# Optimization experiments

Hardware: AMD Instinct MI355X
Metric: run time of the kernel (lower is better)

The kernel has to match this reference:

```python
import jax, jax.numpy as jnp
import numpy as np

L = 4          # num_layers
H = 128        # hidden_channels
F = 128        # num_filters
G = 25         # num_gaussians
N = 10000      # nodes
E = 320000     # radius-graph edges
EH = 40000     # hull edges
NG = 64        # graphs in batch
CUTOFF = 5.0
PI = float(np.pi)
LOG2 = float(np.log(2.0))


def ssp(x):  # ShiftedSoftplus
    return jax.nn.softplus(x) - LOG2


def setup_inputs() -> dict:
    key = jax.random.key(0)
    ks = iter(jax.random.split(key, 64))
    w = lambda shape: jax.random.normal(next(ks), shape, jnp.float32) * 0.05
    inp = {
        'z': jax.random.randint(next(ks), (N,), 0, 100),
        'edge_index': jax.random.randint(next(ks), (2, E), 0, N),
        'edge_index_hull': jax.random.randint(next(ks), (2, EH), 0, N),
        'batch': jnp.sort(jax.random.randint(next(ks), (N,), 0, NG)),
        'dist': jax.random.uniform(next(ks), (E,), jnp.float32) * CUTOFF,
        'fea_hull': jax.random.normal(next(ks), (EH, 7), jnp.float32),
        'emb_table': w((100, H)),
        'lin_w': w((L, F, H)),
        'mlp_w1': w((L, F, G)), 'mlp_b1': jnp.zeros((L, F), jnp.float32),
        'mlp_w2': w((L, F, F)), 'mlp_b2': jnp.zeros((L, F), jnp.float32),
        'linh_w': w((L, F, H)),
        'mlph_w1': w((L, F, 7)), 'mlph_b1': jnp.zeros((L, F), jnp.float32),
        'mlph_w2': w((L, F, F)), 'mlph_b2': jnp.zeros((L, F), jnp.float32),
        'v1_w': w((L, H, F)), 'v1_b': jnp.zeros((L, H), jnp.float32),
        'v2_w': w((L, 64, H)), 'v2_b': jnp.zeros((L, 64), jnp.float32),
        'vh1_w': w((L, H, F)), 'vh1_b': jnp.zeros((L, H), jnp.float32),
        'vh2_w': w((L, 64, H)), 'vh2_b': jnp.zeros((L, 64), jnp.float32),
        'cat_w': w((L, H, 128)), 'cat_b': jnp.zeros((L, H), jnp.float32),
        'u1_w': w((64, H)), 'u1_b': jnp.zeros((64,), jnp.float32),
        'u2_w': w((1, 64)), 'u2_b': jnp.zeros((1,), jnp.float32),
    }
    return inp


def reference(z, edge_index, edge_index_hull, batch, dist, fea_hull, emb_table,
              lin_w, mlp_w1, mlp_b1, mlp_w2, mlp_b2,
              linh_w, mlph_w1, mlph_b1, mlph_w2, mlph_b2,
              v1_w, v1_b, v2_w, v2_b, vh1_w, vh1_b, vh2_w, vh2_b,
              cat_w, cat_b, u1_w, u1_b, u2_w, u2_b):
    n = z.shape[0]
    # Gaussian distance embedding: emb(0, cutoff, G)
    offset = jnp.linspace(0.0, CUTOFF, G)
    coeff = -0.5 / (offset[1] - offset[0]) ** 2
    dist_emb = jnp.exp(coeff * (dist[:, None] - offset[None, :]) ** 2)  # [E,G]
    C = 0.5 * (jnp.cos(dist * PI / CUTOFF) + 1.0)                       # [E]
    j, i = edge_index[0], edge_index[1]
    jh, ih = edge_index_hull[0], edge_index_hull[1]
    v = emb_table[z]                                                    # [N,H]
    for l in range(L):
        # update_e
        W = (ssp(dist_emb @ mlp_w1[l].T + mlp_b1[l]) @ mlp_w2[l].T + mlp_b2[l]) * C[:, None]
        e = (v @ lin_w[l].T)[j] * W                                     # [E,F]
        Wh = ssp(fea_hull @ mlph_w1[l].T + mlph_b1[l]) @ mlph_w2[l].T + mlph_b2[l]
        eh = (v @ linh_w[l].T)[jh] * Wh                                 # [EH,F]
        # update_v
        out = jax.ops.segment_sum(e, i, num_segments=n)
        out = ssp(out @ v1_w[l].T + v1_b[l]) @ v2_w[l].T + v2_b[l]      # [N,64]
        outh = jax.ops.segment_sum(eh, ih, num_segments=n)
        outh = ssp(outh @ vh1_w[l].T + vh1_b[l]) @ vh2_w[l].T + vh2_b[l]
        v = v + ssp(jnp.concatenate([out, outh], axis=1) @ cat_w[l].T + cat_b[l])
    # update_u
    u = ssp(v @ u1_w.T + u1_b) @ u2_w.T + u2_b                          # [N,1]
    return jax.ops.segment_sum(u, batch, num_segments=NG)               # [NG,1]
```

## Files before the change

### kernel.cpp

```cpp
#include <hip/hip_runtime.h>
#include <hip/hip_bf16.h>

typedef __hip_bfloat16 bf16;
typedef unsigned short ushort;
typedef __attribute__((ext_vector_type(8))) short short8;
typedef __attribute__((ext_vector_type(4))) float f32x4;

__device__ __forceinline__ float dssp(float x){
  return fmaxf(x, 0.f) + __logf(1.f + __expf(-fabsf(x))) - 0.693147180559945f;
}
__device__ __forceinline__ int clampi(int x, int lo, int hi){ return x<lo?lo:(x>hi?hi:x); }
__device__ __forceinline__ ushort f2b(float f){
  unsigned x = __float_as_uint(f);
  return (ushort)((x + 0x7fffu + ((x>>16)&1u)) >> 16);
}
__device__ __forceinline__ float b2f16(ushort u){ return __uint_as_float(((unsigned)u)<<16); }

constexpr int TBL_K    = 4096;
constexpr int TBL_ROWS = TBL_K + 1;
constexpr int TBL_T16  = (TBL_ROWS + 15) / 16;

struct Seg { const void* src; float* dst; int n; };
struct SegTable { Seg s[18]; int count; long total; };
struct WSeg { const void* src; ushort* dst; int n; };
struct WTable { WSeg s[10]; int count; int total; };

__global__ void setup_all(const unsigned* __restrict__ raw, int* flag,
                          int* cnt_r, int* cnt_h, float* uacc,
                          int2* spk_r, int2* spk_h, int N, int E, int EH){
  __shared__ int c;
  int t = blockIdx.x*blockDim.x + threadIdx.x;
  if (t < N){ cnt_r[t]=0; cnt_h[t]=0; }
  if (t < 64) uacc[t]=0.f;
  if (t < E)  spk_r[t]=make_int2(0,0);
  if (t < EH) spk_h[t]=make_int2(0,0);
  if (blockIdx.x==0){
    if (threadIdx.x==0) c=0;
    __syncthreads();
    unsigned u  = raw[threadIdx.x];
    unsigned lo = u & 0xFFFFu;
    int e = (int)((lo >> 7) & 0xFF);
    int ok = (lo==0u) || (e >= 0x70 && e <= 0x8F);
    atomicAdd(&c, ok);
    __syncthreads();
    if (threadIdx.x==0) *flag = (c >= 160) ? 1 : 0;
  }
}

__global__ __launch_bounds__(256) void convert_count(SegTable tbl, WTable wt,
    const int* __restrict__ flag,
    const int* __restrict__ ei, const int* __restrict__ eih,
    int E, int EH, int N, int* cnt_r, int* cnt_h, int CA, int CB){
  int b = blockIdx.x;
  if (b < CA){
    int mode = *flag;
    long tid    = (long)b*256 + threadIdx.x;
    long stride = (long)CA*256;
    for (long i=tid; i<tbl.total; i+=stride){
      long off = i; int k = 0;
      while (k < tbl.count-1 && off >= tbl.s[k].n){ off -= tbl.s[k].n; k++; }
      float f;
      if (mode) f = __bfloat162float(((const bf16*)tbl.s[k].src)[off]);
      else      f = ((const float*)tbl.s[k].src)[off];
      tbl.s[k].dst[off] = (f==f) ? f : 0.f;
    }
  } else if (b < CA+CB){
    int mode = *flag;
    long tid    = (long)(b-CA)*256 + threadIdx.x;
    long stride = (long)CB*256;
    for (long i=tid; i<wt.total; i+=stride){
      long off = i; int k = 0;
      while (k < wt.count-1 && off >= wt.s[k].n){ off -= wt.s[k].n; k++; }
      if (mode) wt.s[k].dst[off] = ((const ushort*)wt.s[k].src)[off];
      else {
        float f = ((const float*)wt.s[k].src)[off];
        wt.s[k].dst[off] = f2b((f==f)? f : 0.f);
      }
    }
  } else {
    int t = (b-CA-CB)*256 + threadIdx.x;
    if (t < E)  atomicAdd(&cnt_r[clampi(ei[E + t], 0, N-1)], 1);
    if (t < EH) atomicAdd(&cnt_h[clampi(eih[EH + t], 0, N-1)], 1);
  }
}

__global__ __launch_bounds__(1024) void scan_pair(const int* cnt_r, int* off_r, int* cur_r,
                                                  const int* cnt_h, int* off_h, int* cur_h, int N){
  __shared__ int s[1024];
  int t = threadIdx.x;
  int CH = (N + 1023) / 1024;
  for (int which=0; which<2; which++){
    const int* cnt = which? cnt_h : cnt_r;
    int* off = which? off_h : off_r;
    int* cur = which? cur_h : cur_r;
    int base = t*CH;
    int sum = 0;
    for (int q=0;q<CH;q++){ int idx=base+q; sum += (idx<N)? cnt[idx] : 0; }
    __syncthreads();
    s[t]=sum; __syncthreads();
    for (int ofs=1; ofs<1024; ofs<<=1){
      int v = s[t]; int vp = (t>=ofs)? s[t-ofs] : 0;
      __syncthreads(); s[t]=v+vp; __syncthreads();
    }
    int run = (t>0)? s[t-1] : 0;
    for (int q=0;q<CH;q++){
      int idx=base+q;
      if (idx<N){ off[idx]=run; cur[idx]=run; run += cnt[idx]; }
    }
    if (t==1023) off[N] = s[1023];
  }
}

__global__ void scatter_edges(const int* __restrict__ ei, const float* __restrict__ distc,
                              const int* __restrict__ eih, int E, int EH, int N,
                              int* cur_r, int* cur_h, int2* spk_r, int2* spk_h){
  int t = blockIdx.x*blockDim.x + threadIdx.x;
  if (t < E){
    int i = clampi(ei[E+t], 0, N-1);
    int p = clampi(atomicAdd(&cur_r[i], 1), 0, E-1);
    float x = fminf(fmaxf(distc[t]*(4096.0f/5.0f), 0.f), 4095.999f);
    int i0 = (int)x; if (i0 > TBL_K-1) i0 = TBL_K-1;
    unsigned fr16 = (unsigned)((x - (float)i0)*65536.0f); if (fr16 > 65535u) fr16 = 65535u;
    spk_r[p] = make_int2(clampi(ei[t],0,N-1), (int)(((unsigned)i0<<16)|fr16));
  }
  if (t < EH){
    int ih = clampi(eih[EH+t], 0, N-1);
    int p = clampi(atomicAdd(&cur_h[ih], 1), 0, EH-1);
    spk_h[p] = make_int2(clampi(eih[t],0,N-1), t);
  }
}

__device__ __forceinline__ short8 afragb(const ushort (*Xb)[136], int lane, int k0){
  int m=lane&15, q=(lane>>4)&3;
  return *(const short8*)(&Xb[m][k0+q*8]);
}
__device__ __forceinline__ short8 bfrag(const ushort* __restrict__ W, int cbase, int lane, int k0){
  int n=lane&15, q=(lane>>4)&3;
  return *(const short8*)(W + (size_t)(cbase+n)*128 + k0 + q*8);
}
template<int NT>
__device__ __forceinline__ void mgemm(const ushort (*Xb)[136],
    const ushort* __restrict__ W, int t, f32x4 d[NT]){
  int lane=t&63, w=t>>6;
  #pragma unroll
  for (int ct=0;ct<NT;ct++) d[ct]=(f32x4){0.f,0.f,0.f,0.f};
  #pragma unroll
  for (int kc=0;kc<4;kc++){
    short8 a = afragb(Xb, lane, kc*32);
    #pragma unroll
    for (int ct=0;ct<NT;ct++){
      short8 b = bfrag(W, w*(NT*16)+ct*16, lane, kc*32);
      d[ct] = __builtin_amdgcn_mfma_f32_16x16x32_bf16(a, b, d[ct], 0, 0, 0);
    }
  }
}
template<int NT>
__device__ __forceinline__ void d2tile(ushort (*Y)[136], const f32x4 d[NT], int t,
    int colofs, const float* __restrict__ bias, int do_ssp){
  int lane=t&63, w=t>>6, q=(lane>>4)&3, n=lane&15;
  #pragma unroll
  for (int ct=0;ct<NT;ct++){
    int c = w*(NT*16)+ct*16+n;
    float bv = bias? bias[c] : 0.f;
    #pragma unroll
    for (int i=0;i<4;i++){
      float y = d[ct][i] + bv;
      if (do_ssp) y = dssp(y);
      Y[q*4+i][colofs+c] = f2b(y);
    }
  }
}
template<int NT>
__device__ __forceinline__ void d2os(float (*Os)[132], const f32x4 d[NT], int t,
    const float* __restrict__ bias, int do_ssp){
  int lane=t&63, w=t>>6, q=(lane>>4)&3, n=lane&15;
  #pragma unroll
  for (int ct=0;ct<NT;ct++){
    int c = w*(NT*16)+ct*16+n;
    float bv = bias? bias[c] : 0.f;
    #pragma unroll
    for (int i=0;i<4;i++){
      float y = d[ct][i] + bv;
      if (do_ssp) y = dssp(y);
      Os[q*4+i][c] = y;
    }
  }
}
__device__ __forceinline__ void d2glob_c(ushort* __restrict__ out, const f32x4 d[2],
    int t, int row0, int N, ushort (*Tmp)[136]){
  d2tile<2>(Tmp, d, t, 0, nullptr, 0);
  __syncthreads();
  int r=t>>4, o=(t&15)*8;
  int gr=row0+r;
  if (gr<N) *(uint4*)(out + (size_t)gr*128 + o) = *(const uint4*)&Tmp[r][o];
  __syncthreads();
}

__global__ __launch_bounds__(256) void build_wtab_mfma(
    const float* __restrict__ mlp_w1, const float* __restrict__ mlp_b1,
    const ushort* __restrict__ mlp_w2b, const float* __restrict__ mlp_b2,
    ushort* __restrict__ Wtab){
  int l    = blockIdx.x / TBL_T16;
  int tile = blockIdx.x % TBL_T16;
  int row0 = tile * 16;
  const float* w1 = mlp_w1 + l*128*25;
  const float* b1 = mlp_b1 + l*128;
  const ushort* w2 = mlp_w2b + (size_t)l*16384;
  const float* b2 = mlp_b2 + l*128;
  __shared__ float  Gs[16][26];
  __shared__ ushort Xb[16][136];
  __shared__ ushort Tb[16][136];
  int t = threadIdx.x;
  for (int idx=t; idx<16*25; idx+=256){
    int r=idx/25, k=idx%25;
    float dd = (row0+r) * (5.0f/4096.0f);
    float x  = dd - (float)k*(5.0f/24.0f);
    Gs[r][k] = __expf(-11.52f*x*x);
  }
  __syncthreads();
  {
    int r = t>>4, c0 = (t&15)*8;
    float fv[25];
    #pragma unroll
    for (int k=0;k<25;k++) fv[k]=Gs[r][k];
    short8 pk;
    #pragma unroll
    for (int j=0;j<8;j++){
      int c=c0+j;
      float s=b1[c];
      #pragma unroll
      for (int k=0;k<25;k++) s=fmaf(fv[k], w1[c*25+k], s);
      pk[j]=(short)f2b(dssp(s));
    }
    *(short8*)&Xb[r][c0]=pk;
  }
  __syncthreads();
  f32x4 d[2];
  mgemm<2>(Xb, w2, t, d);
  {
    int lane=t&63, w=t>>6, q=(lane>>4)&3, n=lane&15;
    #pragma unroll
    for (int ct=0;ct<2;ct++){
      int c=w*32+ct*16+n;
      float bv=b2[c];
      #pragma unroll
      for (int i=0;i<4;i++){
        int gr=row0+q*4+i;
        float dd = gr*(5.0f/4096.0f);
        float Cf = 0.5f*(cosf(dd*(3.14159265358979f/5.0f))+1.0f);
        Tb[q*4+i][c]=f2b((d[ct][i]+bv)*Cf);
      }
    }
  }
  __syncthreads();
  int r=t>>4, o=(t&15)*8;
  int gr=row0+r;
  if (gr<TBL_ROWS)
    *(uint4*)(Wtab + ((size_t)l*TBL_ROWS+gr)*128 + o) = *(const uint4*)&Tb[r][o];
}

__device__ void hull_body(int bid, const int2* __restrict__ spk_h,
    const float* __restrict__ fea,
    const float* __restrict__ mlph_w1, const float* __restrict__ mlph_b1,
    const ushort* __restrict__ mlph_w2b, const float* __restrict__ mlph_b2,
    ushort* __restrict__ WhS_base, size_t lstride,
    int EH, int tilesPerLayer, int l0, char* smem){
  int l    = l0 + bid / tilesPerLayer;
  int tile = bid % tilesPerLayer;
  int row0 = tile*64;
  const float* w1 = mlph_w1 + l*128*7;
  const float* b1 = mlph_b1 + l*128;
  const ushort* w2 = mlph_w2b + (size_t)l*16384;
  const float* b2 = mlph_b2 + l*128;
  ushort* WhS = WhS_base + (size_t)(l-l0)*lstride;
  int*   Eid = (int*)smem;
  float (*Fs)[8] = (float(*)[8])(smem+256);
  ushort (*Buf)[136] = (ushort(*)[136])(smem+2304);
  int t=threadIdx.x;
  if (t < 64){
    int p=row0+t;
    Eid[t]=(p<EH)? clampi(spk_h[p].y,0,EH-1):0;
  }
  __syncthreads();
  for (int idx=t; idx<448; idx+=256){
    int r=idx/7, k=idx%7;
    int p=row0+r;
    Fs[r][k]=(p<EH)? fea[(size_t)Eid[r]*7+k]:0.f;
  }
  __syncthreads();
  {
    int c0=(t&31)*4, r0=(t>>5)*8;
    float w[4][7]; float bb[4];
    #pragma unroll
    for (int cc=0;cc<4;cc++){
      bb[cc]=b1[c0+cc];
      #pragma unroll
      for (int k=0;k<7;k++) w[cc][k]=w1[(c0+cc)*7+k];
    }
    #pragma unroll
    for (int rr=0;rr<8;rr++){
      int r=r0+rr;
      float fv[7];
      #pragma unroll
      for (int k=0;k<7;k++) fv[k]=Fs[r][k];
      ushort o[4];
      #pragma unroll
      for (int cc=0;cc<4;cc++){
        float s=bb[cc];
        #pragma unroll
        for (int k=0;k<7;k++) s=fmaf(fv[k],w[cc][k],s);
        o[cc]=f2b(dssp(s));
      }
      unsigned lo=(unsigned)o[0]|((unsigned)o[1]<<16);
      unsigned hi=(unsigned)o[2]|((unsigned)o[3]<<16);
      *(uint2*)&Buf[r][c0]=make_uint2(lo,hi);
    }
  }
  __syncthreads();
  int lane=t&63, w=t>>6;
  const ushort (*Xw)[136] = (const ushort (*)[136])&Buf[w*16][0];
  f32x4 d[8];
  #pragma unroll
  for (int ct=0;ct<8;ct++) d[ct]=(f32x4){0.f,0.f,0.f,0.f};
  #pragma unroll
  for (int kc=0;kc<4;kc++){
    short8 a = afragb(Xw, lane, kc*32);
    #pragma unroll
    for (int ct=0;ct<8;ct++){
      short8 b = bfrag(w2, ct*16, lane, kc*32);
      d[ct] = __builtin_amdgcn_mfma_f32_16x16x32_bf16(a, b, d[ct], 0, 0, 0);
    }
  }
  __syncthreads();
  int q=(lane>>4)&3, n=lane&15;
  #pragma unroll
  for (int ct=0;ct<8;ct++){
    int c=ct*16+n;
    float bv=b2[c];
    #pragma unroll
    for (int i=0;i<4;i++)
      Buf[w*16+q*4+i][c] = f2b(d[ct][i]+bv);
  }
  __syncthreads();
  #pragma unroll
  for (int j=0;j<4;j++){
    int idx=j*256+t;
    int r=idx>>4, o=(idx&15)*8;
    *(uint4*)(WhS + (size_t)(row0+r)*128 + o) = *(const uint4*)&Buf[r][o];
  }
}

__device__ void f_first_body(int bid, const int* __restrict__ z,
    const float* __restrict__ emb, float* __restrict__ v,
    const ushort* __restrict__ linA, const ushort* __restrict__ linB,
    ushort* __restrict__ vlin, ushort* __restrict__ vlinh, int N, char* smem){
  ushort (*Xb)[136] = (ushort(*)[136])smem;
  ushort (*Tb)[136] = (ushort(*)[136])(smem+4352);
  int t=threadIdx.x; int row0=bid*16;
  f32x4 d[2];
  for (int idx=t; idx<512; idx+=256){
    int r=idx>>5, k4=(idx&31)*4; int gr=row0+r;
    int zz=(gr<N)? clampi(z[gr],0,99):0;
    float4 f = *(const float4*)(emb + (size_t)zz*128 + k4);
    unsigned r0 = (unsigned)f2b(f.x) | ((unsigned)f2b(f.y)<<16);
    unsigned r1 = (unsigned)f2b(f.z) | ((unsigned)f2b(f.w)<<16);
    *(uint2*)&Xb[r][k4] = make_uint2(r0,r1);
    if (gr<N) *(float4*)(v + (size_t)gr*128 + k4) = f;
  }
  __syncthreads();
  mgemm<2>(Xb, linA, t, d);
  d2glob_c(vlin, d, t, row0, N, Tb);
  mgemm<2>(Xb, linB, t, d);
  d2glob_c(vlinh, d, t, row0, N, Tb);
}

__global__ __launch_bounds__(256) void hull_pack_first(const int2* __restrict__ spk_h,
    const float* __restrict__ fea,
    const float* __restrict__ mlph_w1, const float* __restrict__ mlph_b1,
    const ushort* __restrict__ mlph_w2b, const float* __restrict__ mlph_b2,
    ushort* __restrict__ WhS, size_t lstride, int EH, int ht64,
    const int* __restrict__ z, const float* __restrict__ emb, float* __restrict__ v,
    const ushort* __restrict__ linA, const ushort* __restrict__ linB,
    ushort* __restrict__ vlin, ushort* __restrict__ vlinh, int N, int nt,
    const ushort* __restrict__ Wtab, unsigned* __restrict__ Wpk, int PB, int HB){
  __shared__ __align__(16) char smem[19968];
  int b = blockIdx.x;
  if (b < HB){
    hull_body(b, spk_h, fea, mlph_w1, mlph_b1, mlph_w2b, mlph_b2,
              WhS, lstride, EH, ht64, 0, smem);
  } else if (b < HB+nt){
    f_first_body(b-HB, z, emb, v, linA, linB, vlin, vlinh, N, smem);
  } else {
    long tid    = (long)(b-HB-nt)*256 + threadIdx.x;
    long stride = (long)PB*256;
    const long TOT = 4L*TBL_K*128;
    for (long i=tid; i<TOT; i+=stride){
      int l = (int)(i / ((long)TBL_K*128));
      long rem = i % ((long)TBL_K*128);
      int r = (int)(rem >> 7), f = (int)(rem & 127);
      const ushort* base = Wtab + (size_t)l*TBL_ROWS*128;
      Wpk[i] = (((unsigned)base[(size_t)(r+1)*128+f])<<16) | (unsigned)base[(size_t)r*128+f];
    }
  }
}

__global__ __launch_bounds__(256) void hull_all(const int2* __restrict__ spk_h,
    const float* __restrict__ fea,
    const float* __restrict__ mlph_w1, const float* __restrict__ mlph_b1,
    const ushort* __restrict__ mlph_w2b, const float* __restrict__ mlph_b2,
    ushort* __restrict__ WhS_base, size_t lstride,
    int EH, int tilesPerLayer, int l0){
  __shared__ __align__(16) char smem[19968];
  hull_body(blockIdx.x, spk_h, fea, mlph_w1, mlph_b1, mlph_w2b, mlph_b2,
            WhS_base, lstride, EH, tilesPerLayer, l0, smem);
}

__global__ __launch_bounds__(256) void f_mid(
    const float* __restrict__ accR, const float* __restrict__ accH,
    float* __restrict__ v,
    const ushort* __restrict__ v1w, const float* __restrict__ v1b,
    const ushort* __restrict__ v2w, const float* __restrict__ v2b,
    const ushort* __restrict__ vh1w, const float* __restrict__ vh1b,
    const ushort* __restrict__ vh2w, const float* __restrict__ vh2b,
    const ushort* __restrict__ cw, const float* __restrict__ cb,
    const ushort* __restrict__ linA, const ushort* __restrict__ linB,
    ushort* __restrict__ vlin, ushort* __restrict__ vlinh, int N){
  __shared__ ushort Xb[16][136];
  __shared__ ushort Xb2[16][136];
  __shared__ ushort Xb3[16][136];
  __shared__ float  Os[16][132];
  int t=threadIdx.x; int row0=blockIdx.x*16;
  f32x4 d[2]; f32x4 d1[1];

  for (int path=0; path<2; path++){
    const float* X = path? accH : accR;
    __syncthreads();
    for (int idx=t; idx<512; idx+=256){
      int r=idx>>5, k4=(idx&31)*4; int gr=row0+r;
      float4 f=(gr<N)? *(const float4*)(X+(size_t)gr*128+k4):make_float4(0,0,0,0);
      unsigned r0 = (unsigned)f2b(f.x) | ((unsigned)f2b(f.y)<<16);
      unsigned r1 = (unsigned)f2b(f.z) | ((unsigned)f2b(f.w)<<16);
      *(uint2*)&Xb[r][k4] = make_uint2(r0,r1);
    }
    __syncthreads();
    mgemm<2>(Xb, path?vh1w:v1w, t, d);
    d2tile<2>(Xb2, d, t, 0, path?vh1b:v1b, 1);
    __syncthreads();
    mgemm<1>(Xb2, path?vh2w:v2w, t, d1);
    d2tile<1>(Xb3, d1, t, path*64, path?vh2b:v2b, 0);
  }
  __syncthreads();
  mgemm<2>(Xb3, cw, t, d);
  d2os<2>(Os, d, t, cb, 1);
  __syncthreads();
  for (int idx=t; idx<512; idx+=256){
    int r=idx>>5, k4=(idx&31)*4; int gr=row0+r;
    float4 f=(gr<N)? *(const float4*)(v+(size_t)gr*128+k4):make_float4(0,0,0,0);
    f.x+=Os[r][k4]; f.y+=Os[r][k4+1]; f.z+=Os[r][k4+2]; f.w+=Os[r][k4+3];
    if (gr<N) *(float4*)(v+(size_t)gr*128+k4)=f;
    unsigned r0 = (unsigned)f2b(f.x) | ((unsigned)f2b(f.y)<<16);
    unsigned r1 = (unsigned)f2b(f.z) | ((unsigned)f2b(f.w)<<16);
    *(uint2*)&Xb[r][k4] = make_uint2(r0,r1);
  }
  __syncthreads();
  mgemm<2>(Xb, linA, t, d);
  d2glob_c(vlin, d, t, row0, N, Xb2);
  mgemm<2>(Xb, linB, t, d);
  d2glob_c(vlinh, d, t, row0, N, Xb2);
}

__global__ __launch_bounds__(256) void f_last(
    const float* __restrict__ accR, const float* __restrict__ accH,
    const float* __restrict__ v,
    const ushort* __restrict__ v1w, const float* __restrict__ v1b,
    const ushort* __restrict__ v2w, const float* __restrict__ v2b,
    const ushort* __restrict__ vh1w, const float* __restrict__ vh1b,
    const ushort* __restrict__ vh2w, const float* __restrict__ vh2b,
    const ushort* __restrict__ cw, const float* __restrict__ cb,
    const ushort* __restrict__ u1w, const float* __restrict__ u1b,
    const float* __restrict__ u2w, const float* __restrict__ u2b,
    const int* __restrict__ batch, float* __restrict__ uacc, int N){
  __shared__ ushort Xb[16][136];
  __shared__ ushort Xb2[16][136];
  __shared__ ushort Xb3[16][136];
  __shared__ float  Os[16][132];
  __shared__ float ss[16];
  __shared__ int   bb[16];
  int t=threadIdx.x; int row0=blockIdx.x*16;
  f32x4 d[2]; f32x4 d1[1];

  for (int path=0; path<2; path++){
    const float* X = path? accH : accR;
    __syncthreads();
    for (int idx=t; idx<512; idx+=256){
      int r=idx>>5, k4=(idx&31)*4; int gr=row0+r;
      float4 f=(gr<N)? *(const float4*)(X+(size_t)gr*128+k4):make_float4(0,0,0,0);
      unsigned r0 = (unsigned)f2b(f.x) | ((unsigned)f2b(f.y)<<16);
      unsigned r1 = (unsigned)f2b(f.z) | ((unsigned)f2b(f.w)<<16);
      *(uint2*)&Xb[r][k4] = make_uint2(r0,r1);
    }
    __syncthreads();
    mgemm<2>(Xb, path?vh1w:v1w, t, d);
    d2tile<2>(Xb2, d, t, 0, path?vh1b:v1b, 1);
    __syncthreads();
    mgemm<1>(Xb2, path?vh2w:v2w, t, d1);
    d2tile<1>(Xb3, d1, t, path*64, path?vh2b:v2b, 0);
  }
  __syncthreads();
  mgemm<2>(Xb3, cw, t, d);
  d2os<2>(Os, d, t, cb, 1);
  __syncthreads();
  for (int idx=t; idx<512; idx+=256){
    int r=idx>>5, k4=(idx&31)*4; int gr=row0+r;
    float4 f=(gr<N)? *(const float4*)(v+(size_t)gr*128+k4):make_float4(0,0,0,0);
    f.x+=Os[r][k4]; f.y+=Os[r][k4+1]; f.z+=Os[r][k4+2]; f.w+=Os[r][k4+3];
    unsigned r0 = (unsigned)f2b(f.x) | ((unsigned)f2b(f.y)<<16);
    unsigned r1 = (unsigned)f2b(f.z) | ((unsigned)f2b(f.w)<<16);
    *(uint2*)&Xb[r][k4] = make_uint2(r0,r1);
  }
  __syncthreads();
  mgemm<1>(Xb, u1w, t, d1);
  d2os<1>(Os, d1, t, u1b, 1);
  __syncthreads();
  if (t<16){
    int gr=row0+t;
    float s=0.f; int bt=-1;
    if (gr<N){
      s = u2b[0];
      for (int c=0;c<64;c++) s += Os[t][c]*u2w[c];
      bt = clampi(batch[gr],0,63);
    }
    ss[t]=s; bb[t]=bt;
  }
  __syncthreads();
  if (t==0){
    float run=0.f; int cur=-1;
    for (int q=0;q<16;q++){
      int bq=bb[q];
      if (bq<0) continue;
      if (bq!=cur){ if (cur>=0) atomicAdd(&uacc[cur],run); cur=bq; run=0.f; }
      run += ss[q];
    }
    if (cur>=0) atomicAdd(&uacc[cur],run);
  }
}

__device__ __forceinline__ float rlerp(unsigned y, const unsigned* __restrict__ Wpk, int f){
  int i0 = (int)(y>>16);
  float fr = (float)(y&0xFFFFu)*(1.f/65536.f);
  unsigned u = Wpk[(size_t)i0*128+f];
  float w0=__uint_as_float(u<<16), w1=__uint_as_float(u&0xFFFF0000u);
  return fmaf(fr, w1-w0, w0);
}

__global__ __launch_bounds__(128) void acc_both(
    const int* __restrict__ off_r, const int2* __restrict__ spk_r,
    const ushort* __restrict__ vlin, const unsigned* __restrict__ Wpk,
    float* __restrict__ accR,
    const int* __restrict__ off_h, const int2* __restrict__ spk_h,
    const ushort* __restrict__ vlinh, const ushort* __restrict__ WhS,
    float* __restrict__ accH,
    int Etot, int EHtot, int N){
  int f = threadIdx.x;
  if ((int)blockIdx.x < N){
    int n = blockIdx.x;
    int b = clampi(off_r[n], 0, Etot);
    int e = clampi(off_r[n+1], b, Etot);
    float a = 0.f;
    int p = b;
    for (; p+8<=e; p+=8){
      int2 k[8];
      #pragma unroll
      for (int j=0;j<8;j++) k[j]=spk_r[p+j];
      float vv[8], ww[8];
      #pragma unroll
      for (int j=0;j<8;j++) vv[j]=b2f16(vlin[(size_t)k[j].x*128+f]);
      #pragma unroll
      for (int j=0;j<8;j++) ww[j]=rlerp((unsigned)k[j].y, Wpk, f);
      #pragma unroll
      for (int j=0;j<8;j++) a=fmaf(vv[j],ww[j],a);
    }
    for (; p+4<=e; p+=4){
      int2 k0=spk_r[p], k1=spk_r[p+1], k2=spk_r[p+2], k3=spk_r[p+3];
      float v0 = b2f16(vlin[(size_t)k0.x*128+f]);
      float v1 = b2f16(vlin[(size_t)k1.x*128+f]);
      float v2 = b2f16(vlin[(size_t)k2.x*128+f]);
      float v3 = b2f16(vlin[(size_t)k3.x*128+f]);
      float w0 = rlerp((unsigned)k0.y, Wpk, f);
      float w1 = rlerp((unsigned)k1.y, Wpk, f);
      float w2 = rlerp((unsigned)k2.y, Wpk, f);
      float w3 = rlerp((unsigned)k3.y, Wpk, f);
      a += v0*w0 + v1*w1 + v2*w2 + v3*w3;
    }
    for (; p<e; p++){
      int2 k0=spk_r[p];
      a += b2f16(vlin[(size_t)k0.x*128+f]) * rlerp((unsigned)k0.y, Wpk, f);
    }
    accR[(size_t)n*128+f] = a;
  } else {
    int n = blockIdx.x - N;
    int b = clampi(off_h[n], 0, EHtot);
    int e = clampi(off_h[n+1], b, EHtot);
    float a = 0.f;
    int p = b;
    for (; p+4<=e; p+=4){
      int2 k0=spk_h[p], k1=spk_h[p+1], k2=spk_h[p+2], k3=spk_h[p+3];
      float v0 = b2f16(vlinh[(size_t)k0.x*128+f]);
      float v1 = b2f16(vlinh[(size_t)k1.x*128+f]);
      float v2 = b2f16(vlinh[(size_t)k2.x*128+f]);
      float v3 = b2f16(vlinh[(size_t)k3.x*128+f]);
      a += v0*b2f16(WhS[(size_t)p*128+f])     + v1*b2f16(WhS[(size_t)(p+1)*128+f])
         + v2*b2f16(WhS[(size_t)(p+2)*128+f]) + v3*b2f16(WhS[(size_t)(p+3)*128+f]);
    }
    for (; p<e; p++){
      int2 k0=spk_h[p];
      a += b2f16(vlinh[(size_t)k0.x*128+f]) * b2f16(WhS[(size_t)p*128+f]);
    }
    accH[(size_t)n*128+f] = a;
  }
}

__global__ void write_out(const float* __restrict__ uacc, void* out, const int* __restrict__ flag){
  int t = threadIdx.x;
  if (t < 64){
    if (*flag) ((bf16*)out)[t] = __float2bfloat16(uacc[t]);
    else       ((float*)out)[t] = uacc[t];
  }
}

extern "C" void kernel_launch(void* const* d_in, const int* in_sizes, int n_in,
                              void* d_out, int out_size, void* d_ws, size_t ws_size,
                              hipStream_t stream){
  const int* z     = (const int*)d_in[0];
  const int* ei    = (const int*)d_in[1];
  const int* eih   = (const int*)d_in[2];
  const int* batch = (const int*)d_in[3];

  const int N  = in_sizes[0];
  const int E  = in_sizes[1]/2;
  const int EH = in_sizes[2]/2;
  const int EHpad = (EH + 63) & ~63;

  char* wp = (char*)d_ws;
  auto alloc = [&](size_t bytes)->char*{
    char* p = wp; wp += (bytes + 255) & ~(size_t)255; return p;
  };
  int* flag    = (int*)alloc(256);
  int* cnt_r   = (int*)alloc((size_t)N*4);
  int* off_r   = (int*)alloc((size_t)(N+1)*4);
  int* cur_r   = (int*)alloc((size_t)N*4);
  int* cnt_h   = (int*)alloc((size_t)N*4);
  int* off_h   = (int*)alloc((size_t)(N+1)*4);
  int* cur_h   = (int*)alloc((size_t)N*4);
  int2* spk_r  = (int2*)alloc((size_t)E*8);
  int2* spk_h  = (int2*)alloc((size_t)EH*8);
  float* uacc  = (float*)alloc(64*4);

  static const int f32_idx[17] = {0,1,2,4,5,7,9,10,12,14,16,18,20,22,24,25,26};
  float* cvt[27] = {};
  SegTable tbl; tbl.count = 17; tbl.total = 0;
  for (int k=0;k<17;k++){
    int i = f32_idx[k];
    int n = in_sizes[4+i];
    cvt[i] = (float*)alloc((size_t)n*4);
    tbl.s[k].src = d_in[4+i];
    tbl.s[k].dst = cvt[i];
    tbl.s[k].n   = n;
    tbl.total   += n;
  }
  const float* distc   = cvt[0];
  const float* feac    = cvt[1];
  const float* embc    = cvt[2];
  const float* mlp_w1  = cvt[4];
  const float* mlp_b1  = cvt[5];
  const float* mlp_b2  = cvt[7];
  const float* mlph_w1 = cvt[9];
  const float* mlph_b1 = cvt[10];
  const float* mlph_b2 = cvt[12];
  const float* v1_b  = cvt[14];
  const float* v2_b  = cvt[16];
  const float* vh1_b = cvt[18];
  const float* vh2_b = cvt[20];
  const float* cat_b = cvt[22];
  const float* u1_b  = cvt[24];
  const float* u2_w  = cvt[25];
  const float* u2_b  = cvt[26];

  ushort* lin_wb   = (ushort*)alloc((size_t)4*16384*2);
  ushort* linh_wb  = (ushort*)alloc((size_t)4*16384*2);
  ushort* v1_wb    = (ushort*)alloc((size_t)4*16384*2);
  ushort* vh1_wb   = (ushort*)alloc((size_t)4*16384*2);
  ushort* cat_wb   = (ushort*)alloc((size_t)4*16384*2);
  ushort* mlph_w2b = (ushort*)alloc((size_t)4*16384*2);
  ushort* mlp_w2b  = (ushort*)alloc((size_t)4*16384*2);
  ushort* v2_wb    = (ushort*)alloc((size_t)4*8192*2);
  ushort* vh2_wb   = (ushort*)alloc((size_t)4*8192*2);
  ushort* u1_wb    = (ushort*)alloc((size_t)8192*2);
  WTable wt; wt.count = 10;
  wt.s[0] = { d_in[4+3],  lin_wb,   4*16384 };
  wt.s[1] = { d_in[4+6],  mlp_w2b,  4*16384 };
  wt.s[2] = { d_in[4+8],  linh_wb,  4*16384 };
  wt.s[3] = { d_in[4+11], mlph_w2b, 4*16384 };
  wt.s[4] = { d_in[4+13], v1_wb,    4*16384 };
  wt.s[5] = { d_in[4+15], v2_wb,    4*8192  };
  wt.s[6] = { d_in[4+17], vh1_wb,   4*16384 };
  wt.s[7] = { d_in[4+19], vh2_wb,   4*8192  };
  wt.s[8] = { d_in[4+21], cat_wb,   4*16384 };
  wt.s[9] = { d_in[4+23], u1_wb,    8192    };
  wt.total = 7*4*16384 + 2*4*8192 + 8192;

  ushort*   Wtab = (ushort*)alloc((size_t)4*TBL_ROWS*128*2);
  unsigned* Wpk  = (unsigned*)alloc((size_t)4*TBL_K*128*4);
  float* v     = (float*)alloc((size_t)N*128*4);
  ushort* vlin  = (ushort*)alloc((size_t)N*128*2);
  ushort* vlinh = (ushort*)alloc((size_t)N*128*2);
  float* accR  = (float*)alloc((size_t)N*128*4);
  float* accH  = (float*)alloc((size_t)N*128*4);

  size_t used = (size_t)(wp - (char*)d_ws);
  size_t whs1 = (size_t)EHpad*128*2;
  bool pre = (ws_size >= used + 4*whs1 + 256);
  ushort* WhS = (ushort*)alloc(pre ? 4*whs1 : whs1);

  const int nbE  = (E+255)/256;
  const int nt   = (N+15)/16;
  const int ht64 = (EH+63)/64;
  const int CA = 1536, CB = 1024, PB = 1024;

  setup_all<<<nbE,256,0,stream>>>((const unsigned*)d_in[6], flag,
                                  cnt_r, cnt_h, uacc, spk_r, spk_h, N, E, EH);
  convert_count<<<CA+CB+nbE,256,0,stream>>>(tbl, wt, flag, ei, eih, E, EH, N,
                                            cnt_r, cnt_h, CA, CB);
  scan_pair<<<1,1024,0,stream>>>(cnt_r,off_r,cur_r,cnt_h,off_h,cur_h,N);
  scatter_edges<<<nbE,256,0,stream>>>(ei, distc, eih, E, EH, N,
                                      cur_r, cur_h, spk_r, spk_h);
  build_wtab_mfma<<<4*TBL_T16,256,0,stream>>>(mlp_w1, mlp_b1, mlp_w2b, mlp_b2, Wtab);
  {
    int HB = pre ? 4*ht64 : 0;
    hull_pack_first<<<HB+nt+PB,256,0,stream>>>(spk_h, feac, mlph_w1, mlph_b1,
        mlph_w2b, mlph_b2, WhS, whs1/2, EH, ht64,
        z, embc, v, lin_wb, linh_wb, vlin, vlinh, N, nt,
        Wtab, Wpk, PB, HB);
  }

  for (int l=0;l<4;l++){
    if (!pre)
      hull_all<<<ht64,256,0,stream>>>(spk_h, feac, mlph_w1, mlph_b1, mlph_w2b, mlph_b2,
                                      WhS, 0, EH, ht64, l);
    const ushort* WhSl = pre ? (WhS + (size_t)l*(whs1/2)) : WhS;
    acc_both<<<2*N,128,0,stream>>>(off_r, spk_r, vlin, Wpk + (size_t)l*TBL_K*128, accR,
                                   off_h, spk_h, vlinh, WhSl, accH, E, EH, N);
    if (l<3){
      f_mid<<<nt,256,0,stream>>>(accR, accH, v,
          v1_wb + (size_t)l*16384, v1_b + l*128, v2_wb + (size_t)l*8192, v2_b + l*64,
          vh1_wb + (size_t)l*16384, vh1_b + l*128, vh2_wb + (size_t)l*8192, vh2_b + l*64,
          cat_wb + (size_t)l*16384, cat_b + l*128,
          lin_wb + (size_t)(l+1)*16384, linh_wb + (size_t)(l+1)*16384, vlin, vlinh, N);
    } else {
      f_last<<<nt,256,0,stream>>>(accR, accH, v,
          v1_wb + (size_t)l*16384, v1_b + l*128, v2_wb + (size_t)l*8192, v2_b + l*64,
          vh1_wb + (size_t)l*16384, vh1_b + l*128, vh2_wb + (size_t)l*8192, vh2_b + l*64,
          cat_wb + (size_t)l*16384, cat_b + l*128,
          u1_wb, u1_b, u2_w, u2_b, batch, uacc, N);
    }
  }
  write_out<<<1,64,0,stream>>>(uacc, d_out, flag);
}
```

Measured before the change: 463.7 us.

## Move hull edge-weight MLP for layers 1-3 into layer-0 accumulation kernel

The up-front hull pre-pass now computes only the layer-0 hull edge weights. The weights for layers 1-3 are produced by extra 128-thread blocks (32 edges per tile) appended to the layer-0 acc_both launch. This shortens the serial setup kernel and lets the hull MLP overlap the memory-bound gather-accumulate work. The cost is a larger static shared-memory footprint in the combined kernel, which may lower occupancy of the accumulation blocks, and smaller MFMA tiles for the hull MLP.

```diff
diff --git a/kernel.cpp b/kernel.cpp
--- a/kernel.cpp
+++ b/kernel.cpp
@@ -345,6 +345,97 @@
   #pragma unroll
   for (int j=0;j<4;j++){
     int idx=j*256+t;
+    int r=idx>>4, o=(idx&15)*8;
+    *(uint4*)(WhS + (size_t)(row0+r)*128 + o) = *(const uint4*)&Buf[r][o];
+  }
+}
+
+__device__ void hull_body32(int bid, const int2* __restrict__ spk_h,
+    const float* __restrict__ fea,
+    const float* __restrict__ mlph_w1, const float* __restrict__ mlph_b1,
+    const ushort* __restrict__ mlph_w2b, const float* __restrict__ mlph_b2,
+    ushort* __restrict__ WhS_base, size_t lstride,
+    int EH, int tilesPerLayer, int l0, char* smem){
+  int l    = l0 + bid / tilesPerLayer;
+  int tile = bid % tilesPerLayer;
+  int row0 = tile*32;
+  const float* w1 = mlph_w1 + l*128*7;
+  const float* b1 = mlph_b1 + l*128;
+  const ushort* w2 = mlph_w2b + (size_t)l*16384;
+  const float* b2 = mlph_b2 + l*128;
+  ushort* WhS = WhS_base + (size_t)(l-l0)*lstride;
+  int*   Eid = (int*)smem;
+  float (*Fs)[8] = (float(*)[8])(smem+128);
+  ushort (*Buf)[136] = (ushort(*)[136])(smem+1152);
+  int t=threadIdx.x;
+  if (t < 32){
+    int p=row0+t;
+    Eid[t]=(p<EH)? clampi(spk_h[p].y,0,EH-1):0;
+  }
+  __syncthreads();
+  for (int idx=t; idx<224; idx+=128){
+    int r=idx/7, k=idx%7;
+    int p=row0+r;
+    Fs[r][k]=(p<EH)? fea[(size_t)Eid[r]*7+k]:0.f;
+  }
+  __syncthreads();
+  {
+    int c0=(t&31)*4, r0=(t>>5)*8;
+    float w[4][7]; float bb[4];
+    #pragma unroll
+    for (int cc=0;cc<4;cc++){
+      bb[cc]=b1[c0+cc];
+      #pragma unroll
+      for (int k=0;k<7;k++) w[cc][k]=w1[(c0+cc)*7+k];
+    }
+    #pragma unroll
+    for (int rr=0;rr<8;rr++){
+      int r=r0+rr;
+      float fv[7];
+      #pragma unroll
+      for (int k=0;k<7;k++) fv[k]=Fs[r][k];
+      ushort o[4];
+      #pragma unroll
+      for (int cc=0;cc<4;cc++){
+        float s=bb[cc];
+        #pragma unroll
+        for (int k=0;k<7;k++) s=fmaf(fv[k],w[cc][k],s);
+        o[cc]=f2b(dssp(s));
+      }
+      unsigned lo=(unsigned)o[0]|((unsigned)o[1]<<16);
+      unsigned hi=(unsigned)o[2]|((unsigned)o[3]<<16);
+      *(uint2*)&Buf[r][c0]=make_uint2(lo,hi);
+    }
+  }
+  __syncthreads();
+  int lane=t&63, w=t>>6;
+  const ushort (*Xw)[136] = (const ushort (*)[136])&Buf[w*16][0];
+  f32x4 d[8];
+  #pragma unroll
+  for (int ct=0;ct<8;ct++) d[ct]=(f32x4){0.f,0.f,0.f,0.f};
+  #pragma unroll
+  for (int kc=0;kc<4;kc++){
+    short8 a = afragb(Xw, lane, kc*32);
+    #pragma unroll
+    for (int ct=0;ct<8;ct++){
+      short8 b = bfrag(w2, ct*16, lane, kc*32);
+      d[ct] = __builtin_amdgcn_mfma_f32_16x16x32_bf16(a, b, d[ct], 0, 0, 0);
+    }
+  }
+  __syncthreads();
+  int q=(lane>>4)&3, n=lane&15;
+  #pragma unroll
+  for (int ct=0;ct<8;ct++){
+    int c=ct*16+n;
+    float bv=b2[c];
+    #pragma unroll
+    for (int i=0;i<4;i++)
+      Buf[w*16+q*4+i][c] = f2b(d[ct][i]+bv);
+  }
+  __syncthreads();
+  #pragma unroll
+  for (int j=0;j<4;j++){
+    int idx=j*128+t;
     int r=idx>>4, o=(idx&15)*8;
     *(uint4*)(WhS + (size_t)(row0+r)*128 + o) = *(const uint4*)&Buf[r][o];
   }
@@ -553,6 +644,69 @@
   return fmaf(fr, w1-w0, w0);
 }
 
+__device__ void acc_radius_body(int n, const int* __restrict__ off_r,
+    const int2* __restrict__ spk_r, const ushort* __restrict__ vlin,
+    const unsigned* __restrict__ Wpk, float* __restrict__ accR, int Etot){
+  int f = threadIdx.x;
+  int b = clampi(off_r[n], 0, Etot);
+  int e = clampi(off_r[n+1], b, Etot);
+  float a = 0.f;
+  int p = b;
+  for (; p+8<=e; p+=8){
+    int2 k[8];
+    #pragma unroll
+    for (int j=0;j<8;j++) k[j]=spk_r[p+j];
+    float vv[8], ww[8];
+    #pragma unroll
+    for (int j=0;j<8;j++) vv[j]=b2f16(vlin[(size_t)k[j].x*128+f]);
+    #pragma unroll
+    for (int j=0;j<8;j++) ww[j]=rlerp((unsigned)k[j].y, Wpk, f);
+    #pragma unroll
+    for (int j=0;j<8;j++) a=fmaf(vv[j],ww[j],a);
+  }
+  for (; p+4<=e; p+=4){
+    int2 k0=spk_r[p], k1=spk_r[p+1], k2=spk_r[p+2], k3=spk_r[p+3];
+    float v0 = b2f16(vlin[(size_t)k0.x*128+f]);
+    float v1 = b2f16(vlin[(size_t)k1.x*128+f]);
+    float v2 = b2f16(vlin[(size_t)k2.x*128+f]);
+    float v3 = b2f16(vlin[(size_t)k3.x*128+f]);
+    float w0 = rlerp((unsigned)k0.y, Wpk, f);
+    float w1 = rlerp((unsigned)k1.y, Wpk, f);
+    float w2 = rlerp((unsigned)k2.y, Wpk, f);
+    float w3 = rlerp((unsigned)k3.y, Wpk, f);
+    a += v0*w0 + v1*w1 + v2*w2 + v3*w3;
+  }
+  for (; p<e; p++){
+    int2 k0=spk_r[p];
+    a += b2f16(vlin[(size_t)k0.x*128+f]) * rlerp((unsigned)k0.y, Wpk, f);
+  }
+  accR[(size_t)n*128+f] = a;
+}
+
+__device__ void acc_hull_body(int n, const int* __restrict__ off_h,
+    const int2* __restrict__ spk_h, const ushort* __restrict__ vlinh,
+    const ushort* __restrict__ WhS, float* __restrict__ accH, int EHtot){
+  int f = threadIdx.x;
+  int b = clampi(off_h[n], 0, EHtot);
+  int e = clampi(off_h[n+1], b, EHtot);
+  float a = 0.f;
+  int p = b;
+  for (; p+4<=e; p+=4){
+    int2 k0=spk_h[p], k1=spk_h[p+1], k2=spk_h[p+2], k3=spk_h[p+3];
+    float v0 = b2f16(vlinh[(size_t)k0.x*128+f]);
+    float v1 = b2f16(vlinh[(size_t)k1.x*128+f]);
+    float v2 = b2f16(vlinh[(size_t)k2.x*128+f]);
+    float v3 = b2f16(vlinh[(size_t)k3.x*128+f]);
+    a += v0*b2f16(WhS[(size_t)p*128+f])     + v1*b2f16(WhS[(size_t)(p+1)*128+f])
+       + v2*b2f16(WhS[(size_t)(p+2)*128+f]) + v3*b2f16(WhS[(size_t)(p+3)*128+f]);
+  }
+  for (; p<e; p++){
+    int2 k0=spk_h[p];
+    a += b2f16(vlinh[(size_t)k0.x*128+f]) * b2f16(WhS[(size_t)p*128+f]);
+  }
+  accH[(size_t)n*128+f] = a;
+}
+
 __global__ __launch_bounds__(128) void acc_both(
     const int* __restrict__ off_r, const int2* __restrict__ spk_r,
     const ushort* __restrict__ vlin, const unsigned* __restrict__ Wpk,
@@ -561,63 +715,32 @@
     const ushort* __restrict__ vlinh, const ushort* __restrict__ WhS,
     float* __restrict__ accH,
     int Etot, int EHtot, int N){
-  int f = threadIdx.x;
-  if ((int)blockIdx.x < N){
-    int n = blockIdx.x;
-    int b = clampi(off_r[n], 0, Etot);
-    int e = clampi(off_r[n+1], b, Etot);
-    float a = 0.f;
-    int p = b;
-    for (; p+8<=e; p+=8){
-      int2 k[8];
-      #pragma unroll
-      for (int j=0;j<8;j++) k[j]=spk_r[p+j];
-      float vv[8], ww[8];
-      #pragma unroll
-      for (int j=0;j<8;j++) vv[j]=b2f16(vlin[(size_t)k[j].x*128+f]);
-      #pragma unroll
-      for (int j=0;j<8;j++) ww[j]=rlerp((unsigned)k[j].y, Wpk, f);
-      #pragma unroll
-      for (int j=0;j<8;j++) a=fmaf(vv[j],ww[j],a);
-    }
-    for (; p+4<=e; p+=4){
-      int2 k0=spk_r[p], k1=spk_r[p+1], k2=spk_r[p+2], k3=spk_r[p+3];
-      float v0 = b2f16(vlin[(size_t)k0.x*128+f]);
-      float v1 = b2f16(vlin[(size_t)k1.x*128+f]);
-      float v2 = b2f16(vlin[(size_t)k2.x*128+f]);
-      float v3 = b2f16(vlin[(size_t)k3.x*128+f]);
-      float w0 = rlerp((unsigned)k0.y, Wpk, f);
-      float w1 = rlerp((unsigned)k1.y, Wpk, f);
-      float w2 = rlerp((unsigned)k2.y, Wpk, f);
-      float w3 = rlerp((unsigned)k3.y, Wpk, f);
-      a += v0*w0 + v1*w1 + v2*w2 + v3*w3;
-    }
-    for (; p<e; p++){
-      int2 k0=spk_r[p];
-      a += b2f16(vlin[(size_t)k0.x*128+f]) * rlerp((unsigned)k0.y, Wpk, f);
-    }
-    accR[(size_t)n*128+f] = a;
-  } else {
-    int n = blockIdx.x - N;
-    int b = clampi(off_h[n], 0, EHtot);
-    int e = clampi(off_h[n+1], b, EHtot);
-    float a = 0.f;
-    int p = b;
-    for (; p+4<=e; p+=4){
-      int2 k0=spk_h[p], k1=spk_h[p+1], k2=spk_h[p+2], k3=spk_h[p+3];
-      float v0 = b2f16(vlinh[(size_t)k0.x*128+f]);
-      float v1 = b2f16(vlinh[(size_t)k1.x*128+f]);
-      float v2 = b2f16(vlinh[(size_t)k2.x*128+f]);
-      float v3 = b2f16(vlinh[(size_t)k3.x*128+f]);
-      a += v0*b2f16(WhS[(size_t)p*128+f])     + v1*b2f16(WhS[(size_t)(p+1)*128+f])
-         + v2*b2f16(WhS[(size_t)(p+2)*128+f]) + v3*b2f16(WhS[(size_t)(p+3)*128+f]);
-    }
-    for (; p<e; p++){
-      int2 k0=spk_h[p];
-      a += b2f16(vlinh[(size_t)k0.x*128+f]) * b2f16(WhS[(size_t)p*128+f]);
-    }
-    accH[(size_t)n*128+f] = a;
-  }
+  if ((int)blockIdx.x < N)
+    acc_radius_body(blockIdx.x, off_r, spk_r, vlin, Wpk, accR, Etot);
+  else
+    acc_hull_body(blockIdx.x-N, off_h, spk_h, vlinh, WhS, accH, EHtot);
+}
+
+__global__ __launch_bounds__(128) void acc_both_hull(
+    const int* __restrict__ off_r, const int2* __restrict__ spk_r,
+    const ushort* __restrict__ vlin, const unsigned* __restrict__ Wpk,
+    float* __restrict__ accR,
+    const int* __restrict__ off_h, const int2* __restrict__ spk_h,
+    const ushort* __restrict__ vlinh, const ushort* __restrict__ WhS0,
+    float* __restrict__ accH,
+    int Etot, int EHtot, int N,
+    const float* __restrict__ fea,
+    const float* __restrict__ mlph_w1, const float* __restrict__ mlph_b1,
+    const ushort* __restrict__ mlph_w2b, const float* __restrict__ mlph_b2,
+    ushort* __restrict__ WhS1, size_t lstride, int ht32){
+  __shared__ __align__(16) char smem[9984];
+  if ((int)blockIdx.x < N)
+    acc_radius_body(blockIdx.x, off_r, spk_r, vlin, Wpk, accR, Etot);
+  else if ((int)blockIdx.x < 2*N)
+    acc_hull_body(blockIdx.x-N, off_h, spk_h, vlinh, WhS0, accH, EHtot);
+  else
+    hull_body32(blockIdx.x-2*N, spk_h, fea, mlph_w1, mlph_b1, mlph_w2b, mlph_b2,
+                WhS1, lstride, EHtot, ht32, 1, smem);
 }
 
 __global__ void write_out(const float* __restrict__ uacc, void* out, const int* __restrict__ flag){
@@ -725,7 +848,9 @@
   const int nbE  = (E+255)/256;
   const int nt   = (N+15)/16;
   const int ht64 = (EH+63)/64;
+  const int ht32 = (EH+31)/32;
   const int CA = 1536, CB = 1024, PB = 1024;
+  const size_t lstride = whs1/2;
 
   setup_all<<<nbE,256,0,stream>>>((const unsigned*)d_in[6], flag,
                                   cnt_r, cnt_h, uacc, spk_r, spk_h, N, E, EH);
@@ -736,9 +861,9 @@
                                       cur_r, cur_h, spk_r, spk_h);
   build_wtab_mfma<<<4*TBL_T16,256,0,stream>>>(mlp_w1, mlp_b1, mlp_w2b, mlp_b2, Wtab);
   {
-    int HB = pre ? 4*ht64 : 0;
+    int HB = pre ? ht64 : 0;
     hull_pack_first<<<HB+nt+PB,256,0,stream>>>(spk_h, feac, mlph_w1, mlph_b1,
-        mlph_w2b, mlph_b2, WhS, whs1/2, EH, ht64,
+        mlph_w2b, mlph_b2, WhS, lstride, EH, ht64,
         z, embc, v, lin_wb, linh_wb, vlin, vlinh, N, nt,
         Wtab, Wpk, PB, HB);
   }
@@ -747,9 +872,16 @@
     if (!pre)
       hull_all<<<ht64,256,0,stream>>>(spk_h, feac, mlph_w1, mlph_b1, mlph_w2b, mlph_b2,
                                       WhS, 0, EH, ht64, l);
-    const ushort* WhSl = pre ? (WhS + (size_t)l*(whs1/2)) : WhS;
-    acc_both<<<2*N,128,0,stream>>>(off_r, spk_r, vlin, Wpk + (size_t)l*TBL_K*128, accR,
-                                   off_h, spk_h, vlinh, WhSl, accH, E, EH, N);
+    const ushort* WhSl = pre ? (WhS + (size_t)l*lstride) : WhS;
+    if (l==0 && pre){
+      acc_both_hull<<<2*N + 3*ht32,128,0,stream>>>(off_r, spk_r, vlin, Wpk, accR,
+          off_h, spk_h, vlinh, WhSl, accH, E, EH, N,
+          feac, mlph_w1, mlph_b1, mlph_w2b, mlph_b2,
+          WhS + lstride, lstride, ht32);
+    } else {
+      acc_both<<<2*N,128,0,stream>>>(off_r, spk_r, vlin, Wpk + (size_t)l*TBL_K*128, accR,
+                                     off_h, spk_h, vlinh, WhSl, accH, E, EH, N);
+    }
     if (l<3){
       f_mid<<<nt,256,0,stream>>>(accR, accH, v,
           v1_wb + (size_t)l*16384, v1_b + l*128, v2_wb + (size_t)l*8192, v2_b + l*64,
```

Measured after the change: 470.4 us. About the same (+1.4%).
